# Performance work log

Hardware: AMD Instinct MI355X
Metric: run time of the kernel (lower is better)

The kernel has to match this reference:

```python
import jax, jax.numpy as jnp
import numpy as np

ROPE_BASE = 10000.0
NEG_INF = -1e9


def _rope_tables(L, dh, dtype):
    # standard RoPE: inv_freq over half dims, tables shaped [L, dh]
    half = dh // 2
    inv_freq = 1.0 / (ROPE_BASE ** (jnp.arange(0, half, dtype=jnp.float32) * 2.0 / dh))
    freqs = jnp.arange(L, dtype=jnp.float32)[:, None] * inv_freq[None, :]  # [L, half]
    emb = jnp.concatenate([freqs, freqs], axis=-1)  # [L, dh]
    return jnp.cos(emb).astype(dtype), jnp.sin(emb).astype(dtype)


def _apply_rope(t, cos, sin):
    # t: [B, H, L, dh]; rotate-half convention
    dh = t.shape[-1]
    t1, t2 = t[..., : dh // 2], t[..., dh // 2:]
    rot = jnp.concatenate([-t2, t1], axis=-1)
    return t * cos[None, None] + rot * sin[None, None]


def setup_inputs() -> dict:
    key = jax.random.key(0)
    ks = jax.random.split(key, 7)
    B, L, D, nh = 2, 2048, 2048, 16
    s = 0.02
    return {
        "x": jax.random.normal(ks[0], (B, L, D), dtype=jnp.float32),
        "Wq": jax.random.normal(ks[1], (D, 2 * D), dtype=jnp.float32) * s,
        "Wk": jax.random.normal(ks[2], (D, D), dtype=jnp.float32) * s,
        "Wv": jax.random.normal(ks[3], (D, D), dtype=jnp.float32) * s,
        "Wl": jax.random.normal(ks[4], (D, nh), dtype=jnp.float32) * s,
        "bl": jnp.zeros((nh,), dtype=jnp.float32),
        "Wo": jax.random.normal(ks[5], (D, D), dtype=jnp.float32) * s,
    }


def reference(x, Wq, Wk, Wv, Wl, bl, Wo):
    B, L, D = x.shape
    nh = Wl.shape[1]
    dh = D // nh

    q = (x @ Wq).reshape(B, L, 2 * nh, dh).transpose(0, 2, 1, 3)  # [B, 2nh, L, dh]
    k = (x @ Wk).reshape(B, L, nh, dh).transpose(0, 2, 1, 3)      # [B, nh, L, dh]
    v = (x @ Wv).reshape(B, L, nh, dh).transpose(0, 2, 1, 3)      # [B, nh, L, dh]

    cos, sin = _rope_tables(L, dh, x.dtype)
    q = _apply_rope(q, cos, sin)
    k = _apply_rope(k, cos, sin)

    # pair query heads (2i, 2i+1) share k/v head i — avoid repeat_interleave
    qp = q.reshape(B, nh, 2, L, dh)
    scale = 1.0 / jnp.sqrt(jnp.asarray(dh, dtype=x.dtype))
    scores = jnp.einsum("bhpqd,bhkd->bhpqk", qp, k) * scale  # [B, nh, 2, L, L]
    causal = jnp.tril(jnp.ones((L, L), dtype=bool))
    scores = jnp.where(causal[None, None, None], scores, NEG_INF)
    probs = jax.nn.softmax(scores, axis=-1)
    ctx = jnp.einsum("bhpqk,bhkd->bhpqd", probs, v)  # [B, nh, 2, L, dh]

    lam = jax.nn.sigmoid(x @ Wl + bl).transpose(0, 2, 1)[..., None]  # [B, nh, L, 1]
    out = ctx[:, :, 0] - lam * ctx[:, :, 1]  # [B, nh, L, dh]
    out = out.transpose(0, 2, 1, 3).reshape(B, L, D)
    return out @ Wo
```

## Files before the change

kernel.cpp:

```cpp
#include <hip/hip_runtime.h>
#include <cstddef>
#include <cstdint>

#define L_SEQ 2048
#define D_MODEL 2048
#define NH 16
#define DH 128
#define M_ROWS 4096

__device__ __forceinline__ ushort f2bf(float f) {
    union { __bf16 b; ushort u; } v; v.b = (__bf16)f; return v.u;
}
__device__ __forceinline__ float bf2f(ushort h) {
    union { uint32_t u; float f; } v; v.u = ((uint32_t)h) << 16; return v.f;
}
__device__ __forceinline__ float2 bf2f2(uint32_t u) {
    union { uint32_t u; float f; } lo, hi;
    lo.u = u << 16; hi.u = u & 0xffff0000u;
    return make_float2(lo.f, hi.f);
}

__device__ __forceinline__ void gld_lds16(const void* g, void* l) {
    __builtin_amdgcn_global_load_lds(
        (const __attribute__((address_space(1))) void*)g,
        (__attribute__((address_space(3))) void*)l, 16, 0, 0);
}

typedef __bf16  bf16x8 __attribute__((ext_vector_type(8)));
typedef float   f32x4  __attribute__((ext_vector_type(4)));

__global__ __launch_bounds__(256) void cvt_bf16(
    const float* __restrict__ in, ushort* __restrict__ out)
{
    const int i = (blockIdx.x * 256 + threadIdx.x) * 8;
    const float4 a = *(const float4*)&in[i];
    const float4 b = *(const float4*)&in[i + 4];
    uint4 o;
    o.x = (uint)f2bf(a.x) | ((uint)f2bf(a.y) << 16);
    o.y = (uint)f2bf(a.z) | ((uint)f2bf(a.w) << 16);
    o.z = (uint)f2bf(b.x) | ((uint)f2bf(b.y) << 16);
    o.w = (uint)f2bf(b.z) | ((uint)f2bf(b.w) << 16);
    *(uint4*)&out[i] = o;
}

__global__ __launch_bounds__(256) void transpose_cvt(
    const float* __restrict__ W, ushort* __restrict__ Wt, int K, int N)
{
    __shared__ float tile[32][33];
    const int n0 = blockIdx.x * 32, k0 = blockIdx.y * 32;
    const int t = threadIdx.x;
    const int r = t >> 3;
    const int c4 = (t & 7) * 4;
    const float4 v = *(const float4*)&W[(size_t)(k0 + r) * N + n0 + c4];
    tile[r][c4 + 0] = v.x; tile[r][c4 + 1] = v.y;
    tile[r][c4 + 2] = v.z; tile[r][c4 + 3] = v.w;
    __syncthreads();
    ushort4 o;
    o.x = f2bf(tile[c4 + 0][r]);
    o.y = f2bf(tile[c4 + 1][r]);
    o.z = f2bf(tile[c4 + 2][r]);
    o.w = f2bf(tile[c4 + 3][r]);
    *(ushort4*)&Wt[(size_t)(n0 + r) * K + k0 + c4] = o;
}

__global__ __launch_bounds__(256) void rope_table(float2* __restrict__ tab)
{
    const int i = blockIdx.x * 256 + threadIdx.x;
    const int d = i & 63, l = i >> 6;
    const float inv = exp2f(-(float)d * 0.20762050593045857f);
    const float ang = (float)l * inv;
    float s, c;
    sincosf(ang, &s, &c);
    tab[i] = make_float2(c, s);
}

__global__ __launch_bounds__(256) void rope_k(
    ushort* __restrict__ T, const float2* __restrict__ tab)
{
    const int idx = blockIdx.x * 256 + threadIdx.x;
    const int d2   = (idx & 31) * 2;
    const int head = (idx >> 5) & 15;
    const int row  = idx >> 9;
    const int l    = row & (L_SEQ - 1);
    const size_t base = (size_t)row * 2048 + head * 128 + d2;
    const uint a = *(const uint*)&T[base];
    const uint b = *(const uint*)&T[base + 64];
    const float2 t0 = bf2f2(a);
    const float2 t1 = bf2f2(b);
    const float2 cs0 = tab[l * 64 + d2];
    const float2 cs1 = tab[l * 64 + d2 + 1];
    const float o0x = t0.x * cs0.x - t1.x * cs0.y;
    const float o0y = t0.y * cs1.x - t1.y * cs1.y;
    const float o1x = t1.x * cs0.x + t0.x * cs0.y;
    const float o1y = t1.y * cs1.x + t0.y * cs1.y;
    *(uint*)&T[base]      = (uint)f2bf(o0x) | ((uint)f2bf(o0y) << 16);
    *(uint*)&T[base + 64] = (uint)f2bf(o1x) | ((uint)f2bf(o1y) << 16);
}

template <int MODE>
__global__ __launch_bounds__(256) void gemm_bf16(
    const ushort* __restrict__ A, const ushort* __restrict__ Bt,
    void* __restrict__ Cv, int M, int N, int K)
{
    __shared__ __align__(16) ushort As[128 * 32];
    __shared__ __align__(16) ushort Bs[128 * 32];
    const int bm = blockIdx.y * 128;
    const int bn = blockIdx.x * 128;
    const int t = threadIdx.x;
    const int w = t >> 6, lane = t & 63;
    const int wm = (w & 1) * 64;
    const int wn = (w >> 1) * 64;

    const int srow = t >> 2;
    const int scol = (t & 3) * 8;
    const ushort* Ag  = A  + (size_t)(bm + srow) * K + scol;
    const ushort* Ag2 = A  + (size_t)(bm + 64 + srow) * K + scol;
    const ushort* Bg  = Bt + (size_t)(bn + srow) * K + scol;
    const ushort* Bg2 = Bt + (size_t)(bn + 64 + srow) * K + scol;
    ushort* Asl  = &As[(size_t)t * 8];
    ushort* Asl2 = &As[(size_t)(t + 256) * 8];
    ushort* Bsl  = &Bs[(size_t)t * 8];
    ushort* Bsl2 = &Bs[(size_t)(t + 256) * 8];

    const int fr = lane & 15;
    const int fq = (lane >> 4) * 8;
    const ushort* Abase = &As[(size_t)(wm + fr) * 32 + fq];
    const ushort* Bbase = &Bs[(size_t)(wn + fr) * 32 + fq];

    f32x4 acc[4][4] = {};

    for (int k0 = 0; k0 < K; k0 += 32) {
        __syncthreads();
        gld_lds16(Ag + k0, Asl);
        gld_lds16(Ag2 + k0, Asl2);
        gld_lds16(Bg + k0, Bsl);
        gld_lds16(Bg2 + k0, Bsl2);
        __syncthreads();
        bf16x8 a[4], b[4];
        #pragma unroll
        for (int i = 0; i < 4; ++i) {
            a[i] = *(const bf16x8*)(Abase + (size_t)i * 16 * 32);
            b[i] = *(const bf16x8*)(Bbase + (size_t)i * 16 * 32);
        }
        #pragma unroll
        for (int mt = 0; mt < 4; ++mt)
            #pragma unroll
            for (int nt = 0; nt < 4; ++nt)
                acc[mt][nt] = __builtin_amdgcn_mfma_f32_16x16x32_bf16(
                    a[mt], b[nt], acc[mt][nt], 0, 0, 0);
    }

    const int crow = (lane >> 4) * 4;
    const int ccol = lane & 15;
    #pragma unroll
    for (int mt = 0; mt < 4; ++mt) {
        #pragma unroll
        for (int nt = 0; nt < 4; ++nt) {
            if (MODE == 3) {
                const size_t row = bm + wm + mt * 16 + crow;
                const size_t col = bn + wn + nt * 16 + ccol;
                ushort4 o4;
                o4.x = f2bf(acc[mt][nt][0]); o4.y = f2bf(acc[mt][nt][1]);
                o4.z = f2bf(acc[mt][nt][2]); o4.w = f2bf(acc[mt][nt][3]);
                *(ushort4*)&((ushort*)Cv)[
                    ((row >> 11) * 16 + (col >> 7)) * (size_t)(128 * 2048)
                    + (col & 127) * 2048 + (row & 2047)] = o4;
            } else {
                #pragma unroll
                for (int reg = 0; reg < 4; ++reg) {
                    const size_t row = bm + wm + mt * 16 + crow + reg;
                    const size_t col = bn + wn + nt * 16 + ccol;
                    if (MODE == 1) {
                        ((ushort*)Cv)[row * N + col] = f2bf(acc[mt][nt][reg]);
                    } else {
                        ((float*)Cv)[row * N + col] = acc[mt][nt][reg];
                    }
                }
            }
        }
    }
}

__global__ __launch_bounds__(256) void lam_kernel(
    const float* __restrict__ X, const float* __restrict__ Wl,
    const float* __restrict__ bl, float* __restrict__ Lam)
{
    const int idx  = blockIdx.x * 256 + threadIdx.x;
    const int hh   = idx & 15;
    const int part = (idx >> 4) & 1;
    const int m    = idx >> 5;
    const float* xr = X + (size_t)m * D_MODEL + part * 1024;
    const float* wl = Wl + (size_t)(part * 1024) * NH;
    float acc = 0.0f;
    for (int d = 0; d < 1024; d += 4) {
        const float4 xv = *(const float4*)&xr[d];
        acc += xv.x * wl[(d + 0) * NH + hh];
        acc += xv.y * wl[(d + 1) * NH + hh];
        acc += xv.z * wl[(d + 2) * NH + hh];
        acc += xv.w * wl[(d + 3) * NH + hh];
    }
    acc += __shfl_xor(acc, 16);
    if (part == 0) {
        acc += bl[hh];
        Lam[(size_t)m * NH + hh] = 1.0f / (1.0f + expf(-acc));
    }
}

__global__ __launch_bounds__(256, 2) void attn_mfma(
    const ushort* __restrict__ Qb, const ushort* __restrict__ Kb,
    const ushort* __restrict__ Vtg, const float* __restrict__ Lam,
    const float2* __restrict__ Rtab, ushort* __restrict__ OutB)
{
    __shared__ __align__(16) ushort lds[27136];
    ushort* K_sh  = lds;
    ushort* Vt_sh = lds + 8704;
    ushort* P_sh  = lds + 17920;

    const int h  = blockIdx.y;
    const int b  = blockIdx.z;
    const int pt = blockIdx.x;
    const int t  = threadIdx.x;
    const int w = t >> 6, lane = t & 63;
    const int colL = lane & 15, quad = lane >> 4;
    const int p = w >> 1, slot = w & 1;
    ushort* Pw = P_sh + w * (32 * 72);

    const ushort* Kgbase = Kb  + (size_t)(b * 2048) * 2048 + h * 128;
    const ushort* Vgbase = Vtg + (size_t)((b * 16 + h) * 128) * 2048;
    const float scale2 = 0.12751744f;

    for (int ph = 0; ph < 2; ++ph) {
        const int qt  = ph ? pt : 31 - pt;
        const int q0  = qt * 64;
        const int r0w = q0 + slot * 32;

        bf16x8 qf[2][4];
        #pragma unroll
        for (int g = 0; g < 2; ++g) {
            const int l = r0w + g * 16 + colL;
            const ushort* Qr = Qb + (size_t)(b * 2048 + l) * 4096
                             + (2 * h + p) * 128 + quad * 8;
            ushort raw[4][8];
            #pragma unroll
            for (int c = 0; c < 4; ++c)
                *(uint4*)raw[c] = *(const uint4*)&Qr[c * 32];
            const float2* tb = Rtab + l * 64 + quad * 8;
            ushort o[4][8];
            #pragma unroll
            for (int c = 0; c < 2; ++c)
                #pragma unroll
                for (int j = 0; j < 8; ++j) {
                    const float2 cs = tb[c * 32 + j];
                    const float a  = bf2f(raw[c][j]);
                    const float bb = bf2f(raw[c + 2][j]);
                    o[c][j]     = f2bf(a * cs.x - bb * cs.y);
                    o[c + 2][j] = f2bf(bb * cs.x + a * cs.y);
                }
            #pragma unroll
            for (int c = 0; c < 4; ++c)
                qf[g][c] = *(const bf16x8*)o[c];
        }

        f32x4 ctx[2][8] = {};
        float m2[2][4] = {{-1e30f,-1e30f,-1e30f,-1e30f},
                          {-1e30f,-1e30f,-1e30f,-1e30f}};
        float li[2][4] = {};

        for (int kt = 0; kt <= qt; ++kt) {
            const int kt0 = kt * 64;
            __syncthreads();
            {
                uint4 kvr[4], vvr[4];
                #pragma unroll
                for (int i = 0; i < 4; ++i) {
                    const int c = t + i * 256;
                    kvr[i] = *(const uint4*)&Kgbase[(size_t)(kt0 + (c >> 4)) * 2048 + (c & 15) * 8];
                    vvr[i] = *(const uint4*)&Vgbase[(size_t)(c >> 3) * 2048 + kt0 + (c & 7) * 8];
                }
                #pragma unroll
                for (int i = 0; i < 4; ++i) {
                    const int c = t + i * 256;
                    *(uint4*)&K_sh[(c >> 4) * 136 + (c & 15) * 8] = kvr[i];
                    *(uint4*)&Vt_sh[(c >> 3) * 72 + (c & 7) * 8]  = vvr[i];
                }
            }
            __syncthreads();

            f32x4 sc2[2][4] = {};
            __builtin_amdgcn_s_setprio(1);
            #pragma unroll
            for (int c = 0; c < 4; ++c)
                #pragma unroll
                for (int nt = 0; nt < 4; ++nt) {
                    const bf16x8 kf = *(const bf16x8*)
                        &K_sh[(nt * 16 + colL) * 136 + c * 32 + quad * 8];
                    sc2[0][nt] = __builtin_amdgcn_mfma_f32_16x16x32_bf16(
                        qf[0][c], kf, sc2[0][nt], 0, 0, 0);
                    sc2[1][nt] = __builtin_amdgcn_mfma_f32_16x16x32_bf16(
                        qf[1][c], kf, sc2[1][nt], 0, 0, 0);
                }
            __builtin_amdgcn_s_setprio(0);

            const bool dmask = (kt == qt);
            #pragma unroll
            for (int g = 0; g < 2; ++g)
                #pragma unroll
                for (int reg = 0; reg < 4; ++reg) {
                    const int row = r0w + g * 16 + quad * 4 + reg;
                    float s[4];
                    #pragma unroll
                    for (int nt = 0; nt < 4; ++nt) {
                        float v = sc2[g][nt][reg] * scale2;
                        if (dmask && (kt0 + nt * 16 + colL > row)) v = -1e9f;
                        s[nt] = v;
                    }
                    float mx = fmaxf(fmaxf(s[0], s[1]), fmaxf(s[2], s[3]));
                    #pragma unroll
                    for (int off = 8; off >= 1; off >>= 1)
                        mx = fmaxf(mx, __shfl_xor(mx, off));
                    if (__any(mx > m2[g][reg] + 11.0f)) {
                        const float mnew  = fmaxf(m2[g][reg], mx);
                        const float alpha = exp2f(m2[g][reg] - mnew);
                        li[g][reg] *= alpha;
                        m2[g][reg] = mnew;
                        #pragma unroll
                        for (int nt2 = 0; nt2 < 8; ++nt2)
                            ctx[g][nt2][reg] *= alpha;
                    }
                    float rs = 0.f;
                    #pragma unroll
                    for (int nt = 0; nt < 4; ++nt) {
                        const float pv = exp2f(s[nt] - m2[g][reg]);
                        s[nt] = pv;
                        rs += pv;
                    }
                    #pragma unroll
                    for (int off = 8; off >= 1; off >>= 1)
                        rs += __shfl_xor(rs, off);
                    li[g][reg] += rs;
                    #pragma unroll
                    for (int nt = 0; nt < 4; ++nt)
                        Pw[(g * 16 + quad * 4 + reg) * 72 + nt * 16 + colL]
                            = f2bf(s[nt]);
                }

            __builtin_amdgcn_s_setprio(1);
            #pragma unroll
            for (int c2 = 0; c2 < 2; ++c2) {
                const bf16x8 pf0 = *(const bf16x8*)
                    &Pw[colL * 72 + c2 * 32 + quad * 8];
                const bf16x8 pf1 = *(const bf16x8*)
                    &Pw[(16 + colL) * 72 + c2 * 32 + quad * 8];
                #pragma unroll
                for (int nt2 = 0; nt2 < 8; ++nt2) {
                    const bf16x8 vf = *(const bf16x8*)
                        &Vt_sh[(nt2 * 16 + colL) * 72 + c2 * 32 + quad * 8];
                    ctx[0][nt2] = __builtin_amdgcn_mfma_f32_16x16x32_bf16(
                        pf0, vf, ctx[0][nt2], 0, 0, 0);
                    ctx[1][nt2] = __builtin_amdgcn_mfma_f32_16x16x32_bf16(
                        pf1, vf, ctx[1][nt2], 0, 0, 0);
                }
            }
            __builtin_amdgcn_s_setprio(0);
        }

        float invl[2][4];
        #pragma unroll
        for (int g = 0; g < 2; ++g)
            #pragma unroll
            for (int reg = 0; reg < 4; ++reg)
                invl[g][reg] = 1.0f / li[g][reg];

        float* comb = (float*)lds;
        __syncthreads();
        if (p == 1) {
            #pragma unroll
            for (int g = 0; g < 2; ++g)
                #pragma unroll
                for (int nt2 = 0; nt2 < 8; ++nt2)
                    #pragma unroll
                    for (int reg = 0; reg < 4; ++reg)
                        comb[(slot * 32 + g * 16 + quad * 4 + reg) * 130
                             + nt2 * 16 + colL] = ctx[g][nt2][reg] * invl[g][reg];
        }
        __syncthreads();
        if (p == 0) {
            #pragma unroll
            for (int g = 0; g < 2; ++g)
                #pragma unroll
                for (int reg = 0; reg < 4; ++reg) {
                    const int row = r0w + g * 16 + quad * 4 + reg;
                    const float lamv = Lam[(size_t)(b * 2048 + row) * 16 + h];
                    ushort* orow = OutB + (size_t)(b * 2048 + row) * 2048 + h * 128;
                    #pragma unroll
                    for (int nt2 = 0; nt2 < 8; ++nt2) {
                        const float c1 = comb[(slot * 32 + g * 16 + quad * 4 + reg) * 130
                                              + nt2 * 16 + colL];
                        const float o = ctx[g][nt2][reg] * invl[g][reg] - lamv * c1;
                        orow[nt2 * 16 + colL] = f2bf(o);
                    }
                }
        }
        __syncthreads();
    }
}

extern "C" void kernel_launch(void* const* d_in, const int* in_sizes, int n_in,
                              void* d_out, int out_size, void* d_ws, size_t ws_size,
                              hipStream_t stream)
{
    const float* x  = (const float*)d_in[0];
    const float* Wq = (const float*)d_in[1];
    const float* Wk = (const float*)d_in[2];
    const float* Wv = (const float*)d_in[3];
    const float* Wl = (const float*)d_in[4];
    const float* bl = (const float*)d_in[5];
    const float* Wo = (const float*)d_in[6];
    float* out = (float*)d_out;
    (void)ws_size; (void)in_sizes; (void)n_in; (void)out_size;

    ushort* ws   = (ushort*)d_ws;
    ushort* xb   = ws;
    ushort* Qb16 = xb   + (size_t)8388608;
    ushort* Kb16 = Qb16 + (size_t)16777216;
    ushort* Vtg  = Kb16 + (size_t)8388608;
    ushort* Wqt  = Vtg  + (size_t)8388608;
    ushort* Wkt  = Wqt  + (size_t)8388608;
    ushort* Wvt  = Wkt  + (size_t)4194304;
    ushort* Wot  = Wvt  + (size_t)4194304;
    ushort* OutB = Wot  + (size_t)4194304;
    float*  LamB = (float*)(OutB + (size_t)8388608);
    float2* Rtab = (float2*)(LamB + (size_t)65536);

    cvt_bf16<<<4096, 256, 0, stream>>>(x, xb);
    transpose_cvt<<<dim3(128, 64), 256, 0, stream>>>(Wq, Wqt, 2048, 4096);
    transpose_cvt<<<dim3(64, 64), 256, 0, stream>>>(Wk, Wkt, 2048, 2048);
    transpose_cvt<<<dim3(64, 64), 256, 0, stream>>>(Wv, Wvt, 2048, 2048);
    transpose_cvt<<<dim3(64, 64), 256, 0, stream>>>(Wo, Wot, 2048, 2048);
    lam_kernel<<<512, 256, 0, stream>>>(x, Wl, bl, LamB);
    rope_table<<<512, 256, 0, stream>>>(Rtab);

    gemm_bf16<1><<<dim3(32, 32), 256, 0, stream>>>(xb, Wqt, Qb16, M_ROWS, 4096, D_MODEL);
    gemm_bf16<1><<<dim3(16, 32), 256, 0, stream>>>(xb, Wkt, Kb16, M_ROWS, D_MODEL, D_MODEL);
    gemm_bf16<3><<<dim3(16, 32), 256, 0, stream>>>(xb, Wvt, Vtg, M_ROWS, D_MODEL, D_MODEL);

    rope_k<<<8192, 256, 0, stream>>>(Kb16, Rtab);

    attn_mfma<<<dim3(16, NH, 2), 256, 0, stream>>>(Qb16, Kb16, Vtg, LamB, Rtab, OutB);

    gemm_bf16<0><<<dim3(16, 32), 256, 0, stream>>>(OutB, Wot, out, M_ROWS, D_MODEL, D_MODEL);
}
```

Measured before the change: 661.6 us.

## Prefetch K/V tiles via async global-to-LDS loads with rotating swizzled buffers

The attention kernel now copies K and V tiles straight from global memory into LDS with `global_load_lds`, instead of loading them into registers and then storing them. It uses three rotating LDS buffers so the next tile's loads are issued after QK^T and overlap with the softmax and PV phases. Row padding is replaced with an XOR swizzle to avoid bank conflicts without extra space. The aim is to hide global load latency and cut register pressure and VGPR traffic, at the cost of more LDS per block (about 67KB), which could limit occupancy.

Result: faster. 632.7 us (-4.4%).

```diff
diff --git a/kernel.cpp b/kernel.cpp
--- a/kernel.cpp
+++ b/kernel.cpp
@@ -211,10 +211,8 @@
     const ushort* __restrict__ Vtg, const float* __restrict__ Lam,
     const float2* __restrict__ Rtab, ushort* __restrict__ OutB)
 {
-    __shared__ __align__(16) ushort lds[27136];
-    ushort* K_sh  = lds;
-    ushort* Vt_sh = lds + 8704;
-    ushort* P_sh  = lds + 17920;
+    __shared__ __align__(16) ushort lds[33792];
+    ushort* P_sh = lds + 24576;
 
     const int h  = blockIdx.y;
     const int b  = blockIdx.z;
@@ -229,6 +227,27 @@
     const ushort* Vgbase = Vtg + (size_t)((b * 16 + h) * 128) * 2048;
     const float scale2 = 0.12751744f;
 
+    auto stageK = [&](ushort* dst, int kt0) {
+        #pragma unroll
+        for (int j = 0; j < 4; ++j) {
+            const int idx = j * 256 + t;
+            const int kr = idx >> 4;
+            const int kg = t & 15;
+            gld_lds16(Kgbase + (size_t)(kt0 + kr) * 2048 + ((kg ^ (kr & 15)) << 3),
+                      dst + (size_t)idx * 8);
+        }
+    };
+    auto stageV = [&](ushort* dst, int kt0) {
+        #pragma unroll
+        for (int j = 0; j < 4; ++j) {
+            const int idx = j * 256 + t;
+            const int vr = idx >> 3;
+            const int vg = t & 7;
+            gld_lds16(Vgbase + (size_t)vr * 2048 + kt0 + ((vg ^ (vr & 7)) << 3),
+                      dst + (size_t)idx * 8);
+        }
+    };
+
     for (int ph = 0; ph < 2; ++ph) {
         const int qt  = ph ? pt : 31 - pt;
         const int q0  = qt * 64;
@@ -266,25 +285,16 @@
                           {-1e30f,-1e30f,-1e30f,-1e30f}};
         float li[2][4] = {};
 
+        ushort* Kc = lds;
+        ushort* Vc = lds + 8192;
+        ushort* Fr = lds + 16384;
+
+        stageK(Kc, 0);
+        stageV(Vc, 0);
+        __syncthreads();
+
         for (int kt = 0; kt <= qt; ++kt) {
             const int kt0 = kt * 64;
-            __syncthreads();
-            {
-                uint4 kvr[4], vvr[4];
-                #pragma unroll
-                for (int i = 0; i < 4; ++i) {
-                    const int c = t + i * 256;
-                    kvr[i] = *(const uint4*)&Kgbase[(size_t)(kt0 + (c >> 4)) * 2048 + (c & 15) * 8];
-                    vvr[i] = *(const uint4*)&Vgbase[(size_t)(c >> 3) * 2048 + kt0 + (c & 7) * 8];
-                }
-                #pragma unroll
-                for (int i = 0; i < 4; ++i) {
-                    const int c = t + i * 256;
-                    *(uint4*)&K_sh[(c >> 4) * 136 + (c & 15) * 8] = kvr[i];
-                    *(uint4*)&Vt_sh[(c >> 3) * 72 + (c & 7) * 8]  = vvr[i];
-                }
-            }
-            __syncthreads();
 
             f32x4 sc2[2][4] = {};
             __builtin_amdgcn_s_setprio(1);
@@ -292,14 +302,21 @@
             for (int c = 0; c < 4; ++c)
                 #pragma unroll
                 for (int nt = 0; nt < 4; ++nt) {
+                    const int krow = nt * 16 + colL;
                     const bf16x8 kf = *(const bf16x8*)
-                        &K_sh[(nt * 16 + colL) * 136 + c * 32 + quad * 8];
+                        &Kc[krow * 128 + (((c * 4 + quad) ^ (krow & 15)) << 3)];
                     sc2[0][nt] = __builtin_amdgcn_mfma_f32_16x16x32_bf16(
                         qf[0][c], kf, sc2[0][nt], 0, 0, 0);
                     sc2[1][nt] = __builtin_amdgcn_mfma_f32_16x16x32_bf16(
                         qf[1][c], kf, sc2[1][nt], 0, 0, 0);
                 }
             __builtin_amdgcn_s_setprio(0);
+
+            __syncthreads();
+            if (kt < qt) {
+                stageK(Fr, kt0 + 64);
+                stageV(Kc, kt0 + 64);
+            }
 
             const bool dmask = (kt == qt);
             #pragma unroll
@@ -353,8 +370,9 @@
                     &Pw[(16 + colL) * 72 + c2 * 32 + quad * 8];
                 #pragma unroll
                 for (int nt2 = 0; nt2 < 8; ++nt2) {
+                    const int vrow = nt2 * 16 + colL;
                     const bf16x8 vf = *(const bf16x8*)
-                        &Vt_sh[(nt2 * 16 + colL) * 72 + c2 * 32 + quad * 8];
+                        &Vc[vrow * 64 + (((c2 * 4 + quad) ^ (vrow & 7)) << 3)];
                     ctx[0][nt2] = __builtin_amdgcn_mfma_f32_16x16x32_bf16(
                         pf0, vf, ctx[0][nt2], 0, 0, 0);
                     ctx[1][nt2] = __builtin_amdgcn_mfma_f32_16x16x32_bf16(
@@ -362,6 +380,9 @@
                 }
             }
             __builtin_amdgcn_s_setprio(0);
+
+            __syncthreads();
+            ushort* tmp = Fr; Fr = Vc; Vc = Kc; Kc = tmp;
         }
 
         float invl[2][4];
```
